# Optimization experiments

Measured on AMD Instinct MI355X. Metric: run time of the kernel, lower is better.

Reference implementation:

```python
import jax, jax.numpy as jnp
import numpy as np

EMBED_DIM = 256
MAX_SENT_NUM = 50


def position_embeddings(max_sent_num, embed_dim):
    # pos[p, i] = sin(p / 200**(i/embed_dim))
    p = jnp.arange(max_sent_num, dtype=jnp.float32)[:, None]
    i = jnp.arange(embed_dim, dtype=jnp.float32)[None, :] / embed_dim
    return jnp.sin(p / jnp.power(200.0, i))


def setup_inputs() -> dict:
    key = jax.random.key(0)
    k1, k2, k3, k4 = jax.random.split(key, 4)
    B, S, N, E = 8192, 50, 20, EMBED_DIM
    return {
        "encoded_sents": jax.random.normal(k1, (B, S, E), dtype=jnp.float32),
        "entities": jax.random.normal(k2, (B, N, E), dtype=jnp.float32),
        "attn_matrix": jax.random.normal(k3, (E, E), dtype=jnp.float32) * 0.05,
        "dense_w": jax.random.normal(k4, (E, 1), dtype=jnp.float32) * 0.05,
        "dense_b": jnp.zeros((1,), dtype=jnp.float32),
    }


def reference(encoded_sents, entities, attn_matrix, dense_w, dense_b):
    B, S, E = encoded_sents.shape
    pos = position_embeddings(MAX_SENT_NUM, E)[:S]          # [S, E]
    x = encoded_sents + pos[None, :, :]                      # [B, S, E]

    # attention over previous sentences; query = last sentence's hidden state
    query = x[:, -1, :]                                      # [B, E]
    logits = jnp.einsum("be,bse->bs", query, x)              # [B, S]
    coef = jax.nn.softmax(logits, axis=1)                    # [B, S]
    attn_hidden = jnp.einsum("bs,bse->be", coef, x)          # [B, E]

    # entity attention: (query @ W) elementwise-weighted sum over entities (no softmax)
    q_ent = attn_hidden @ attn_matrix                        # [B, E]
    attn_ent = jnp.einsum("be,bne->be", q_ent, entities)     # [B, E] (sum over n)

    return jax.nn.sigmoid(attn_ent @ dense_w + dense_b)      # [B, 1]
```

## Files before the change

kernel.cpp:

```cpp
#include <hip/hip_runtime.h>
#include <math.h>

#define BATCH 8192
#define SENTS 50
#define ED    256
#define NENT  20
#define BB    16

#define SENT_BLOCKS BATCH
#define ENT_BLOCKS  (BATCH / 4)

#define RATE_K 0.0298588132413075f

typedef float f4 __attribute__((ext_vector_type(4)));

__global__ __launch_bounds__(256) void fat_kernel(
    const float* __restrict__ sents, const float* __restrict__ entities,
    const float* __restrict__ dense_w,
    float* __restrict__ h_out, float* __restrict__ m_out)
{
    __shared__ __align__(16) float hp[4][ED];
    __shared__ float md[4][2];

    int t = threadIdx.x;

    if (blockIdx.x < SENT_BLOCKS) {
        int b = blockIdx.x;
        int c = t & 63;
        int r = t >> 6;
        bool has13 = (r < 2);

        const f4* s4 = (const f4*)(sents + (size_t)b * SENTS * ED);

        f4 qv = __builtin_nontemporal_load(&s4[49 * 64 + c]);
        f4 xv[13];
        #pragma unroll
        for (int k = 0; k < 12; ++k)
            xv[k] = __builtin_nontemporal_load(&s4[(r + 4 * k) * 64 + c]);
        if (has13) xv[12] = __builtin_nontemporal_load(&s4[(r + 48) * 64 + c]);

        f4 rate;
        rate.x = exp2f(-(float)(4 * c + 0) * RATE_K);
        rate.y = exp2f(-(float)(4 * c + 1) * RATE_K);
        rate.z = exp2f(-(float)(4 * c + 2) * RATE_K);
        rate.w = exp2f(-(float)(4 * c + 3) * RATE_K);

        f4 q;
        q.x = qv.x + __sinf(49.f * rate.x);
        q.y = qv.y + __sinf(49.f * rate.y);
        q.z = qv.z + __sinf(49.f * rate.z);
        q.w = qv.w + __sinf(49.f * rate.w);

        f4 x[13];
        float lg[13];
        #pragma unroll
        for (int k = 0; k < 13; ++k) {
            if (k < 12 || has13) {
                float fs = (float)(r + 4 * k);
                x[k].x = xv[k].x + __sinf(fs * rate.x);
                x[k].y = xv[k].y + __sinf(fs * rate.y);
                x[k].z = xv[k].z + __sinf(fs * rate.z);
                x[k].w = xv[k].w + __sinf(fs * rate.w);
                float p = x[k].x * q.x + x[k].y * q.y + x[k].z * q.z + x[k].w * q.w;
                p += __shfl_xor(p, 1);
                p += __shfl_xor(p, 2);
                p += __shfl_xor(p, 4);
                p += __shfl_xor(p, 8);
                p += __shfl_xor(p, 16);
                p += __shfl_xor(p, 32);
                lg[k] = p;
            }
        }

        float mr = lg[0];
        #pragma unroll
        for (int k = 1; k < 13; ++k)
            if (k < 12 || has13) mr = fmaxf(mr, lg[k]);

        float dr = 0.f;
        f4 hacc = (f4)0.f;
        #pragma unroll
        for (int k = 0; k < 13; ++k) {
            if (k < 12 || has13) {
                float w = __expf(lg[k] - mr);
                dr += w;
                hacc.x += w * x[k].x; hacc.y += w * x[k].y;
                hacc.z += w * x[k].z; hacc.w += w * x[k].w;
            }
        }

        *(f4*)&hp[r][4 * c] = hacc;
        if (c == 0) { md[r][0] = mr; md[r][1] = dr; }
        __syncthreads();

        float m0 = md[0][0], d0 = md[0][1];
        float m1 = md[1][0], d1 = md[1][1];
        float m2 = md[2][0], d2 = md[2][1];
        float m3 = md[3][0], d3 = md[3][1];
        float M  = fmaxf(fmaxf(m0, m1), fmaxf(m2, m3));
        float s0 = __expf(m0 - M), s1 = __expf(m1 - M);
        float s2 = __expf(m2 - M), s3 = __expf(m3 - M);
        float dd = s0 * d0 + s1 * d1 + s2 * d2 + s3 * d3;
        float hv = s0 * hp[0][t] + s1 * hp[1][t] + s2 * hp[2][t] + s3 * hp[3][t];
        h_out[(size_t)b * ED + t] = hv / dd;
    } else {
        int b = (blockIdx.x - SENT_BLOCKS) * 4 + (t >> 6);
        int c = t & 63;

        const f4* e4 = (const f4*)(entities + (size_t)b * NENT * ED);

        f4 a[NENT];
        #pragma unroll
        for (int n = 0; n < NENT; ++n)
            a[n] = __builtin_nontemporal_load(&e4[n * 64 + c]);

        f4 s = (f4)0.f;
        #pragma unroll
        for (int n = 0; n < NENT; ++n) s += a[n];

        f4 w4 = ((const f4*)dense_w)[c];
        s *= w4;
        ((f4*)(m_out + (size_t)b * ED))[c] = s;
    }
}

__global__ __launch_bounds__(256) void bilinear_kernel(
    const float* __restrict__ hws, const float* __restrict__ mws,
    const float* __restrict__ A, const float* __restrict__ dense_b,
    float* __restrict__ out)
{
    __shared__ __align__(16) float hl[BB][ED];
    __shared__ float ml[BB][ED];
    __shared__ float part[BB][ED];

    int t  = threadIdx.x;
    int b0 = blockIdx.x * BB;

    for (int i = 0; i < BB; ++i) {
        hl[i][t] = hws[(size_t)(b0 + i) * ED + t];
        ml[i][t] = mws[(size_t)(b0 + i) * ED + t];
    }
    __syncthreads();

    float acc[BB];
    #pragma unroll
    for (int i = 0; i < BB; ++i) acc[i] = 0.f;

    for (int ep = 0; ep < ED; ep += 4) {
        float a0 = A[(ep + 0) * ED + t];
        float a1 = A[(ep + 1) * ED + t];
        float a2 = A[(ep + 2) * ED + t];
        float a3 = A[(ep + 3) * ED + t];
        #pragma unroll
        for (int i = 0; i < BB; ++i) {
            float4 hv = *(const float4*)&hl[i][ep];
            acc[i] += hv.x * a0 + hv.y * a1 + hv.z * a2 + hv.w * a3;
        }
    }

    #pragma unroll
    for (int i = 0; i < BB; ++i) part[i][t] = acc[i] * ml[i][t];
    __syncthreads();

    int lane = t & 63, w = t >> 6;
    float bias = dense_b[0];
    for (int i = w; i < BB; i += 4) {
        float v = part[i][lane] + part[i][lane + 64] + part[i][lane + 128] + part[i][lane + 192];
        for (int off = 32; off >= 1; off >>= 1) v += __shfl_xor(v, off);
        if (lane == 0) out[b0 + i] = 1.f / (1.f + __expf(-(v + bias)));
    }
}

__global__ __launch_bounds__(256) void fused_kernel(
    const float* __restrict__ sents, const float* __restrict__ entities,
    const float* __restrict__ A, const float* __restrict__ dense_w,
    const float* __restrict__ dense_b, float* __restrict__ out)
{
    __shared__ __align__(16) float xs[SENTS][ED + 4];
    __shared__ float logit_s[64];
    __shared__ float coef[64];
    __shared__ __align__(16) float harr[ED];
    __shared__ float marr[ED];
    __shared__ float red[4];

    int t    = threadIdx.x;
    int b    = blockIdx.x;
    int lane = t & 63;
    int w    = t >> 6;

    float rate = exp2f(-(float)t * RATE_K);
    const float* sp = sents + (size_t)b * SENTS * ED;
    for (int s = 0; s < SENTS; ++s)
        xs[s][t] = sp[s * ED + t] + sinf((float)s * rate);
    __syncthreads();

    float4 q = *(const float4*)&xs[SENTS - 1][lane * 4];
    for (int s = w; s < SENTS; s += 4) {
        float4 v = *(const float4*)&xs[s][lane * 4];
        float p = v.x * q.x + v.y * q.y + v.z * q.z + v.w * q.w;
        p += __shfl_down(p, 32);
        p += __shfl_down(p, 16);
        p += __shfl_down(p, 8);
        p += __shfl_down(p, 4);
        p += __shfl_down(p, 2);
        p += __shfl_down(p, 1);
        if (lane == 0) logit_s[s] = p;
    }
    __syncthreads();

    if (w == 0) {
        float l = (lane < SENTS) ? logit_s[lane] : -INFINITY;
        float mx = l;
        for (int off = 32; off >= 1; off >>= 1) mx = fmaxf(mx, __shfl_xor(mx, off));
        float ex = (lane < SENTS) ? expf(l - mx) : 0.f;
        float sm = ex;
        for (int off = 32; off >= 1; off >>= 1) sm += __shfl_xor(sm, off);
        if (lane < SENTS) coef[lane] = ex / sm;
    }
    __syncthreads();

    float h = 0.f;
    #pragma unroll
    for (int s = 0; s < SENTS; ++s) h += coef[s] * xs[s][t];

    const float* ent = entities + (size_t)b * NENT * ED;
    float es = 0.f;
    #pragma unroll
    for (int n = 0; n < NENT; ++n) es += ent[n * ED + t];
    float m = es * dense_w[t];

    harr[t] = h;
    marr[t] = m;
    __syncthreads();

    float acc = 0.f;
    for (int ep = 0; ep < ED; ep += 4) {
        float4 hv = *(const float4*)&harr[ep];
        acc += hv.x * A[(ep + 0) * ED + t];
        acc += hv.y * A[(ep + 1) * ED + t];
        acc += hv.z * A[(ep + 2) * ED + t];
        acc += hv.w * A[(ep + 3) * ED + t];
    }
    float val = acc * marr[t];
    val += __shfl_down(val, 32);
    val += __shfl_down(val, 16);
    val += __shfl_down(val, 8);
    val += __shfl_down(val, 4);
    val += __shfl_down(val, 2);
    val += __shfl_down(val, 1);
    if (lane == 0) red[w] = val;
    __syncthreads();
    if (t == 0) {
        float tot = red[0] + red[1] + red[2] + red[3];
        out[b] = 1.f / (1.f + expf(-(tot + dense_b[0])));
    }
}

extern "C" void kernel_launch(void* const* d_in, const int* in_sizes, int n_in,
                              void* d_out, int out_size, void* d_ws, size_t ws_size,
                              hipStream_t stream) {
    const float* sents    = (const float*)d_in[0];
    const float* entities = (const float*)d_in[1];
    const float* A        = (const float*)d_in[2];
    const float* dense_w  = (const float*)d_in[3];
    const float* dense_b  = (const float*)d_in[4];
    float* out = (float*)d_out;

    size_t hm_bytes = (size_t)BATCH * ED * sizeof(float);
    size_t need = 2 * hm_bytes;

    if (ws_size >= need) {
        float* hws = (float*)d_ws;
        float* mws = (float*)((char*)d_ws + hm_bytes);
        fat_kernel<<<SENT_BLOCKS + ENT_BLOCKS, 256, 0, stream>>>(
            sents, entities, dense_w, hws, mws);
        bilinear_kernel<<<BATCH / BB, 256, 0, stream>>>(hws, mws, A, dense_b, out);
    } else {
        fused_kernel<<<BATCH, 256, 0, stream>>>(sents, entities, A, dense_w, dense_b, out);
    }
}
```

Measured before the change: 132.8 us.

## Fuse sentence attention, entity sum and bilinear into one per-batch kernel

Replaces the two-kernel pipeline (fat kernel writing h and m to workspace, then a batched bilinear kernel) with a single kernel per batch row. Each block loads its sentences and entities together, computes the softmax-weighted hidden state and the entity sum, then does the 256x256 matvec against A and the final reduction and sigmoid. This removes the workspace round trip and the second launch. In exchange every block re-reads all of A (256 KB) instead of amortizing it over 16 rows, which leans on cache bandwidth.

```diff
diff --git a/kernel.cpp b/kernel.cpp
--- a/kernel.cpp
+++ b/kernel.cpp
@@ -5,94 +5,107 @@
 #define SENTS 50
 #define ED    256
 #define NENT  20
-#define BB    16
-
-#define SENT_BLOCKS BATCH
-#define ENT_BLOCKS  (BATCH / 4)
 
 #define RATE_K 0.0298588132413075f
 
 typedef float f4 __attribute__((ext_vector_type(4)));
 
-__global__ __launch_bounds__(256) void fat_kernel(
+__global__ __launch_bounds__(256) void fused_all_kernel(
     const float* __restrict__ sents, const float* __restrict__ entities,
-    const float* __restrict__ dense_w,
-    float* __restrict__ h_out, float* __restrict__ m_out)
+    const float* __restrict__ A, const float* __restrict__ dense_w,
+    const float* __restrict__ dense_b, float* __restrict__ out)
 {
     __shared__ __align__(16) float hp[4][ED];
+    __shared__ __align__(16) float ep[4][ED];
+    __shared__ __align__(16) float pp[4][ED];
     __shared__ float md[4][2];
+    __shared__ float hl[ED];
+    __shared__ float ml[ED];
+    __shared__ float wred[4];
 
     int t = threadIdx.x;
+    int c = t & 63;
+    int r = t >> 6;
+    int b = blockIdx.x;
+    bool has13 = (r < 2);
 
-    if (blockIdx.x < SENT_BLOCKS) {
-        int b = blockIdx.x;
-        int c = t & 63;
-        int r = t >> 6;
-        bool has13 = (r < 2);
+    const f4* s4 = (const f4*)(sents + (size_t)b * SENTS * ED);
+    const f4* e4 = (const f4*)(entities + (size_t)b * NENT * ED);
 
-        const f4* s4 = (const f4*)(sents + (size_t)b * SENTS * ED);
+    f4 qv = __builtin_nontemporal_load(&s4[49 * 64 + c]);
+    f4 xv[13];
+    #pragma unroll
+    for (int k = 0; k < 12; ++k)
+        xv[k] = __builtin_nontemporal_load(&s4[(r + 4 * k) * 64 + c]);
+    if (has13) xv[12] = __builtin_nontemporal_load(&s4[(r + 48) * 64 + c]);
+    f4 ev[5];
+    #pragma unroll
+    for (int n = 0; n < 5; ++n)
+        ev[n] = __builtin_nontemporal_load(&e4[(r + 4 * n) * 64 + c]);
+    float wt = dense_w[t];
 
-        f4 qv = __builtin_nontemporal_load(&s4[49 * 64 + c]);
-        f4 xv[13];
-        #pragma unroll
-        for (int k = 0; k < 12; ++k)
-            xv[k] = __builtin_nontemporal_load(&s4[(r + 4 * k) * 64 + c]);
-        if (has13) xv[12] = __builtin_nontemporal_load(&s4[(r + 48) * 64 + c]);
+    f4 rate;
+    rate.x = exp2f(-(float)(4 * c + 0) * RATE_K);
+    rate.y = exp2f(-(float)(4 * c + 1) * RATE_K);
+    rate.z = exp2f(-(float)(4 * c + 2) * RATE_K);
+    rate.w = exp2f(-(float)(4 * c + 3) * RATE_K);
 
-        f4 rate;
-        rate.x = exp2f(-(float)(4 * c + 0) * RATE_K);
-        rate.y = exp2f(-(float)(4 * c + 1) * RATE_K);
-        rate.z = exp2f(-(float)(4 * c + 2) * RATE_K);
-        rate.w = exp2f(-(float)(4 * c + 3) * RATE_K);
+    f4 q;
+    q.x = qv.x + __sinf(49.f * rate.x);
+    q.y = qv.y + __sinf(49.f * rate.y);
+    q.z = qv.z + __sinf(49.f * rate.z);
+    q.w = qv.w + __sinf(49.f * rate.w);
 
-        f4 q;
-        q.x = qv.x + __sinf(49.f * rate.x);
-        q.y = qv.y + __sinf(49.f * rate.y);
-        q.z = qv.z + __sinf(49.f * rate.z);
-        q.w = qv.w + __sinf(49.f * rate.w);
+    f4 x[13];
+    float lg[13];
+    #pragma unroll
+    for (int k = 0; k < 13; ++k) {
+        if (k < 12 || has13) {
+            float fs = (float)(r + 4 * k);
+            x[k].x = xv[k].x + __sinf(fs * rate.x);
+            x[k].y = xv[k].y + __sinf(fs * rate.y);
+            x[k].z = xv[k].z + __sinf(fs * rate.z);
+            x[k].w = xv[k].w + __sinf(fs * rate.w);
+            float p = x[k].x * q.x + x[k].y * q.y + x[k].z * q.z + x[k].w * q.w;
+            p += __shfl_xor(p, 1);
+            p += __shfl_xor(p, 2);
+            p += __shfl_xor(p, 4);
+            p += __shfl_xor(p, 8);
+            p += __shfl_xor(p, 16);
+            p += __shfl_xor(p, 32);
+            lg[k] = p;
+        }
+    }
 
-        f4 x[13];
-        float lg[13];
-        #pragma unroll
-        for (int k = 0; k < 13; ++k) {
-            if (k < 12 || has13) {
-                float fs = (float)(r + 4 * k);
-                x[k].x = xv[k].x + __sinf(fs * rate.x);
-                x[k].y = xv[k].y + __sinf(fs * rate.y);
-                x[k].z = xv[k].z + __sinf(fs * rate.z);
-                x[k].w = xv[k].w + __sinf(fs * rate.w);
-                float p = x[k].x * q.x + x[k].y * q.y + x[k].z * q.z + x[k].w * q.w;
-                p += __shfl_xor(p, 1);
-                p += __shfl_xor(p, 2);
-                p += __shfl_xor(p, 4);
-                p += __shfl_xor(p, 8);
-                p += __shfl_xor(p, 16);
-                p += __shfl_xor(p, 32);
-                lg[k] = p;
-            }
+    float mr = lg[0];
+    #pragma unroll
+    for (int k = 1; k < 13; ++k)
+        if (k < 12 || has13) mr = fmaxf(mr, lg[k]);
+
+    float dr = 0.f;
+    f4 hacc = (f4)0.f;
+    #pragma unroll
+    for (int k = 0; k < 13; ++k) {
+        if (k < 12 || has13) {
+            float w = __expf(lg[k] - mr);
+            dr += w;
+            hacc.x += w * x[k].x; hacc.y += w * x[k].y;
+            hacc.z += w * x[k].z; hacc.w += w * x[k].w;
         }
+    }
 
-        float mr = lg[0];
-        #pragma unroll
-        for (int k = 1; k < 13; ++k)
-            if (k < 12 || has13) mr = fmaxf(mr, lg[k]);
+    f4 es;
+    es.x = ((ev[0].x + ev[1].x) + (ev[2].x + ev[3].x)) + ev[4].x;
+    es.y = ((ev[0].y + ev[1].y) + (ev[2].y + ev[3].y)) + ev[4].y;
+    es.z = ((ev[0].z + ev[1].z) + (ev[2].z + ev[3].z)) + ev[4].z;
+    es.w = ((ev[0].w + ev[1].w) + (ev[2].w + ev[3].w)) + ev[4].w;
 
-        float dr = 0.f;
-        f4 hacc = (f4)0.f;
-        #pragma unroll
-        for (int k = 0; k < 13; ++k) {
-            if (k < 12 || has13) {
-                float w = __expf(lg[k] - mr);
-                dr += w;
-                hacc.x += w * x[k].x; hacc.y += w * x[k].y;
-                hacc.z += w * x[k].z; hacc.w += w * x[k].w;
-            }
-        }
+    *(f4*)&hp[r][4 * c] = hacc;
+    *(f4*)&ep[r][4 * c] = es;
+    if (c == 0) { md[r][0] = mr; md[r][1] = dr; }
+    __syncthreads();
 
-        *(f4*)&hp[r][4 * c] = hacc;
-        if (c == 0) { md[r][0] = mr; md[r][1] = dr; }
-        __syncthreads();
-
+    {
         float m0 = md[0][0], d0 = md[0][1];
         float m1 = md[1][0], d1 = md[1][1];
         float m2 = md[2][0], d2 = md[2][1];
@@ -102,157 +115,37 @@
         float s2 = __expf(m2 - M), s3 = __expf(m3 - M);
         float dd = s0 * d0 + s1 * d1 + s2 * d2 + s3 * d3;
         float hv = s0 * hp[0][t] + s1 * hp[1][t] + s2 * hp[2][t] + s3 * hp[3][t];
-        h_out[(size_t)b * ED + t] = hv / dd;
-    } else {
-        int b = (blockIdx.x - SENT_BLOCKS) * 4 + (t >> 6);
-        int c = t & 63;
-
-        const f4* e4 = (const f4*)(entities + (size_t)b * NENT * ED);
-
-        f4 a[NENT];
-        #pragma unroll
-        for (int n = 0; n < NENT; ++n)
-            a[n] = __builtin_nontemporal_load(&e4[n * 64 + c]);
-
-        f4 s = (f4)0.f;
-        #pragma unroll
-        for (int n = 0; n < NENT; ++n) s += a[n];
-
-        f4 w4 = ((const f4*)dense_w)[c];
-        s *= w4;
-        ((f4*)(m_out + (size_t)b * ED))[c] = s;
-    }
-}
-
-__global__ __launch_bounds__(256) void bilinear_kernel(
-    const float* __restrict__ hws, const float* __restrict__ mws,
-    const float* __restrict__ A, const float* __restrict__ dense_b,
-    float* __restrict__ out)
-{
-    __shared__ __align__(16) float hl[BB][ED];
-    __shared__ float ml[BB][ED];
-    __shared__ float part[BB][ED];
-
-    int t  = threadIdx.x;
-    int b0 = blockIdx.x * BB;
-
-    for (int i = 0; i < BB; ++i) {
-        hl[i][t] = hws[(size_t)(b0 + i) * ED + t];
-        ml[i][t] = mws[(size_t)(b0 + i) * ED + t];
+        hl[t] = hv / dd;
+        ml[t] = ((ep[0][t] + ep[1][t]) + (ep[2][t] + ep[3][t])) * wt;
     }
     __syncthreads();
 
-    float acc[BB];
-    #pragma unroll
-    for (int i = 0; i < BB; ++i) acc[i] = 0.f;
-
-    for (int ep = 0; ep < ED; ep += 4) {
-        float a0 = A[(ep + 0) * ED + t];
-        float a1 = A[(ep + 1) * ED + t];
-        float a2 = A[(ep + 2) * ED + t];
-        float a3 = A[(ep + 3) * ED + t];
-        #pragma unroll
-        for (int i = 0; i < BB; ++i) {
-            float4 hv = *(const float4*)&hl[i][ep];
-            acc[i] += hv.x * a0 + hv.y * a1 + hv.z * a2 + hv.w * a3;
-        }
+    const f4* A4 = (const f4*)A;
+    f4 acc = (f4)0.f;
+    #pragma unroll 8
+    for (int j = 0; j < 64; ++j) {
+        int e = r + 4 * j;
+        float hs = hl[e];
+        f4 av = A4[e * 64 + c];
+        acc.x += hs * av.x; acc.y += hs * av.y;
+        acc.z += hs * av.z; acc.w += hs * av.w;
     }
-
-    #pragma unroll
-    for (int i = 0; i < BB; ++i) part[i][t] = acc[i] * ml[i][t];
+    *(f4*)&pp[r][4 * c] = acc;
     __syncthreads();
 
-    int lane = t & 63, w = t >> 6;
-    float bias = dense_b[0];
-    for (int i = w; i < BB; i += 4) {
-        float v = part[i][lane] + part[i][lane + 64] + part[i][lane + 128] + part[i][lane + 192];
-        for (int off = 32; off >= 1; off >>= 1) v += __shfl_xor(v, off);
-        if (lane == 0) out[b0 + i] = 1.f / (1.f + __expf(-(v + bias)));
-    }
-}
-
-__global__ __launch_bounds__(256) void fused_kernel(
-    const float* __restrict__ sents, const float* __restrict__ entities,
-    const float* __restrict__ A, const float* __restrict__ dense_w,
-    const float* __restrict__ dense_b, float* __restrict__ out)
-{
-    __shared__ __align__(16) float xs[SENTS][ED + 4];
-    __shared__ float logit_s[64];
-    __shared__ float coef[64];
-    __shared__ __align__(16) float harr[ED];
-    __shared__ float marr[ED];
-    __shared__ float red[4];
-
-    int t    = threadIdx.x;
-    int b    = blockIdx.x;
-    int lane = t & 63;
-    int w    = t >> 6;
-
-    float rate = exp2f(-(float)t * RATE_K);
-    const float* sp = sents + (size_t)b * SENTS * ED;
-    for (int s = 0; s < SENTS; ++s)
-        xs[s][t] = sp[s * ED + t] + sinf((float)s * rate);
+    float v = ((pp[0][t] + pp[1][t]) + (pp[2][t] + pp[3][t])) * ml[t];
+    v += __shfl_xor(v, 1);
+    v += __shfl_xor(v, 2);
+    v += __shfl_xor(v, 4);
+    v += __shfl_xor(v, 8);
+    v += __shfl_xor(v, 16);
+    v += __shfl_xor(v, 32);
+    if (c == 0) wred[r] = v;
     __syncthreads();
 
-    float4 q = *(const float4*)&xs[SENTS - 1][lane * 4];
-    for (int s = w; s < SENTS; s += 4) {
-        float4 v = *(const float4*)&xs[s][lane * 4];
-        float p = v.x * q.x + v.y * q.y + v.z * q.z + v.w * q.w;
-        p += __shfl_down(p, 32);
-        p += __shfl_down(p, 16);
-        p += __shfl_down(p, 8);
-        p += __shfl_down(p, 4);
-        p += __shfl_down(p, 2);
-        p += __shfl_down(p, 1);
-        if (lane == 0) logit_s[s] = p;
-    }
-    __syncthreads();
-
-    if (w == 0) {
-        float l = (lane < SENTS) ? logit_s[lane] : -INFINITY;
-        float mx = l;
-        for (int off = 32; off >= 1; off >>= 1) mx = fmaxf(mx, __shfl_xor(mx, off));
-        float ex = (lane < SENTS) ? expf(l - mx) : 0.f;
-        float sm = ex;
-        for (int off = 32; off >= 1; off >>= 1) sm += __shfl_xor(sm, off);
-        if (lane < SENTS) coef[lane] = ex / sm;
-    }
-    __syncthreads();
-
-    float h = 0.f;
-    #pragma unroll
-    for (int s = 0; s < SENTS; ++s) h += coef[s] * xs[s][t];
-
-    const float* ent = entities + (size_t)b * NENT * ED;
-    float es = 0.f;
-    #pragma unroll
-    for (int n = 0; n < NENT; ++n) es += ent[n * ED + t];
-    float m = es * dense_w[t];
-
-    harr[t] = h;
-    marr[t] = m;
-    __syncthreads();
-
-    float acc = 0.f;
-    for (int ep = 0; ep < ED; ep += 4) {
-        float4 hv = *(const float4*)&harr[ep];
-        acc += hv.x * A[(ep + 0) * ED + t];
-        acc += hv.y * A[(ep + 1) * ED + t];
-        acc += hv.z * A[(ep + 2) * ED + t];
-        acc += hv.w * A[(ep + 3) * ED + t];
-    }
-    float val = acc * marr[t];
-    val += __shfl_down(val, 32);
-    val += __shfl_down(val, 16);
-    val += __shfl_down(val, 8);
-    val += __shfl_down(val, 4);
-    val += __shfl_down(val, 2);
-    val += __shfl_down(val, 1);
-    if (lane == 0) red[w] = val;
-    __syncthreads();
     if (t == 0) {
-        float tot = red[0] + red[1] + red[2] + red[3];
-        out[b] = 1.f / (1.f + expf(-(tot + dense_b[0])));
+        float tot = (wred[0] + wred[1]) + (wred[2] + wred[3]);
+        out[b] = 1.f / (1.f + __expf(-(tot + dense_b[0])));
     }
 }
 
@@ -266,16 +159,6 @@
     const float* dense_b  = (const float*)d_in[4];
     float* out = (float*)d_out;
 
-    size_t hm_bytes = (size_t)BATCH * ED * sizeof(float);
-    size_t need = 2 * hm_bytes;
-
-    if (ws_size >= need) {
-        float* hws = (float*)d_ws;
-        float* mws = (float*)((char*)d_ws + hm_bytes);
-        fat_kernel<<<SENT_BLOCKS + ENT_BLOCKS, 256, 0, stream>>>(
-            sents, entities, dense_w, hws, mws);
-        bilinear_kernel<<<BATCH / BB, 256, 0, stream>>>(hws, mws, A, dense_b, out);
-    } else {
-        fused_kernel<<<BATCH, 256, 0, stream>>>(sents, entities, A, dense_w, dense_b, out);
-    }
+    fused_all_kernel<<<BATCH, 256, 0, stream>>>(
+        sents, entities, A, dense_w, dense_b, out);
 }
```

Result: slower. 140.4 us (+5.7%).
